# Optimization experiments

Hardware: AMD Instinct MI355X
Metric: run time of the kernel (lower is better)

The kernel has to match this reference:

```python
import jax, jax.numpy as jnp
import numpy as np


def setup_inputs() -> dict:
    key = jax.random.key(0)
    k1, k2 = jax.random.split(key)
    B, C, H, W = 8, 16, 512, 512
    x = jax.random.normal(k1, (B, C, H, W), dtype=jnp.float32)
    # displacement field in voxel units, channels-first like the torch module
    phi = jax.random.normal(k2, (B, 2, H, W), dtype=jnp.float32) * 3.0
    return {"x": x, "phi": phi}


def _pull2d_wrap(img, disp):
    """img: [B,H,W,C], disp: [B,H,W,2] (displacement in voxels).
    Linear interpolation with circulant ('dft') boundary = wrap via mod."""
    B, H, W, C = img.shape
    gy = jnp.arange(H, dtype=img.dtype)[:, None]   # [H,1]
    gx = jnp.arange(W, dtype=img.dtype)[None, :]   # [1,W]
    cy = disp[..., 0] + gy                          # [B,H,W] sample coords (abs)
    cx = disp[..., 1] + gx
    y0f = jnp.floor(cy)
    x0f = jnp.floor(cx)
    wy = (cy - y0f)[..., None]                      # [B,H,W,1]
    wx = (cx - x0f)[..., None]
    y0 = jnp.mod(y0f.astype(jnp.int32), H)
    x0 = jnp.mod(x0f.astype(jnp.int32), W)
    y1 = jnp.mod(y0 + 1, H)
    x1 = jnp.mod(x0 + 1, W)

    def gather(im, yi, xi):                         # im [H,W,C]; yi,xi [H,W]
        return im[yi, xi]

    g = jax.vmap(gather)
    v00 = g(img, y0, x0)
    v01 = g(img, y0, x1)
    v10 = g(img, y1, x0)
    v11 = g(img, y1, x1)
    top = v00 * (1 - wx) + v01 * wx
    bot = v10 * (1 - wx) + v11 * wx
    return top * (1 - wy) + bot * wy                # [B,H,W,C]


def reference(x, phi):
    # x: [B,C,H,W], phi: [B,2,H,W] -> channels-last, pull, channels-first
    img = jnp.moveaxis(x, 1, -1)
    disp = jnp.moveaxis(phi, 1, -1)
    out = _pull2d_wrap(img, disp)
    return jnp.moveaxis(out, -1, 1)
```

## Files before the change

### kernel.cpp

```cpp
#include <hip/hip_runtime.h>


constexpr int B = 8, C = 16, H = 512, W = 512;
constexpr int HW = H * W;

typedef float    v2f __attribute__((ext_vector_type(2)));
typedef _Float16 v8h __attribute__((ext_vector_type(8)));

__global__ __launch_bounds__(256) void transpose_h_kernel(const float* __restrict__ x,
                                                          v8h* __restrict__ xt8) {
    int idx = blockIdx.x * blockDim.x + threadIdx.x;
    int b   = idx >> 18;
    int rem = idx & ((1 << 18) - 1);
    int pp  = rem >> 1;
    int q8  = rem & 1;
    int p0  = pp * 2;

    const float* src = x + ((size_t)b * C + q8 * 8) * HW + p0;
    v8h o0, o1;
#pragma unroll
    for (int j = 0; j < 8; ++j) {
        v2f c = __builtin_nontemporal_load((const v2f*)(src + (size_t)j * HW));
        o0[j] = (_Float16)c.x;
        o1[j] = (_Float16)c.y;
    }

    v8h* dst = xt8 + ((size_t)b * HW + p0) * 2 + q8;
    dst[0] = o0;
    dst[2] = o1;
}

__global__ __launch_bounds__(256) void gather_h_kernel(const v8h* __restrict__ xt8,
                                                       const float* __restrict__ phi,
                                                       float* __restrict__ out) {
    int idx = blockIdx.x * blockDim.x + threadIdx.x;
    int b   = idx >> 19;
    int rem = idx & (HW * 2 - 1);
    int p   = rem >> 1;
    int q   = rem & 1;
    int h   = p >> 9;
    int w   = p & (W - 1);

    const float* phib = phi + (size_t)b * 2 * HW;
    float cy = __builtin_nontemporal_load(phib + p)      + (float)h;
    float cx = __builtin_nontemporal_load(phib + HW + p) + (float)w;

    float y0f = floorf(cy);
    float x0f = floorf(cx);
    float wy  = cy - y0f;
    float wx  = cx - x0f;

    int y0 = ((int)y0f) & (H - 1);
    int x0 = ((int)x0f) & (W - 1);
    int y1 = (y0 + 1)   & (H - 1);
    int x1 = (x0 + 1)   & (W - 1);

    const v8h* base = xt8 + (size_t)b * HW * 2;
    v8h v00 = base[(y0 * W + x0) * 2 + q];
    v8h v01 = base[(y0 * W + x1) * 2 + q];
    v8h v10 = base[(y1 * W + x0) * 2 + q];
    v8h v11 = base[(y1 * W + x1) * 2 + q];

    float omwx = 1.0f - wx;
    float omwy = 1.0f - wy;

    float* outp = out + ((size_t)b * C + q * 8) * HW + p;
#pragma unroll
    for (int j = 0; j < 8; ++j) {
        float top = (float)v00[j] * omwx + (float)v01[j] * wx;
        float bot = (float)v10[j] * omwx + (float)v11[j] * wx;
        __builtin_nontemporal_store(top * omwy + bot * wy, outp + (size_t)j * HW);
    }
}

__global__ __launch_bounds__(256) void pull_wrap_kernel(const float* __restrict__ x,
                                                        const float* __restrict__ phi,
                                                        float* __restrict__ out) {
    int idx = blockIdx.x * blockDim.x + threadIdx.x;
    if (idx >= B * HW) return;
    int b  = idx >> 18;
    int hw = idx & (HW - 1);
    int h  = hw >> 9;
    int w  = hw & (W - 1);

    const float* phib = phi + (size_t)b * 2 * HW;
    float cy = phib[hw]      + (float)h;
    float cx = phib[HW + hw] + (float)w;

    float y0f = floorf(cy);
    float x0f = floorf(cx);
    float wy  = cy - y0f;
    float wx  = cx - x0f;

    int y0 = ((int)y0f) & (H - 1);
    int x0 = ((int)x0f) & (W - 1);
    int y1 = (y0 + 1)   & (H - 1);
    int x1 = (x0 + 1)   & (W - 1);

    int o00 = y0 * W + x0;
    int o01 = y0 * W + x1;
    int o10 = y1 * W + x0;
    int o11 = y1 * W + x1;

    float omwx = 1.0f - wx;
    float omwy = 1.0f - wy;

    const float* plane = x   + (size_t)b * C * HW;
    float*       outp  = out + (size_t)b * C * HW + hw;

#pragma unroll
    for (int c = 0; c < C; ++c) {
        float v00 = plane[o00];
        float v01 = plane[o01];
        float v10 = plane[o10];
        float v11 = plane[o11];
        float top = v00 * omwx + v01 * wx;
        float bot = v10 * omwx + v11 * wx;
        outp[(size_t)c * HW] = top * omwy + bot * wy;
        plane += HW;
    }
}

extern "C" void kernel_launch(void* const* d_in, const int* in_sizes, int n_in,
                              void* d_out, int out_size, void* d_ws, size_t ws_size,
                              hipStream_t stream) {
    const float* x   = (const float*)d_in[0];
    const float* phi = (const float*)d_in[1];
    float* out = (float*)d_out;

    size_t need = (size_t)B * HW * C * sizeof(_Float16);
    if (d_ws != nullptr && ws_size >= need) {
        dim3 block(256);
        dim3 tgrid((B * (HW / 2) * 2) / 256);
        dim3 ggrid((B * HW * 2) / 256);
        transpose_h_kernel<<<tgrid, block, 0, stream>>>(x, (v8h*)d_ws);
        gather_h_kernel<<<ggrid, block, 0, stream>>>((const v8h*)d_ws, phi, out);
    } else {
        int n = B * HW;
        dim3 block(256);
        dim3 grid((n + 255) / 256);
        pull_wrap_kernel<<<grid, block, 0, stream>>>(x, phi, out);
    }
}
```

Before: 274.4 us.

## Widen transpose to 4 pixels, gather all 16 channels per thread, add XCD swizzle

The transpose kernel now loads float4 and emits four fp16 channel vectors per thread, halving its thread count. The gather kernel has each thread handle all 16 channels of one pixel, so the coordinate and weight math and the phi loads are not repeated across two threads. Both kernels remap block IDs so contiguous work chunks land on the same XCD, which should improve L2 locality for the gathers. Each gather thread now holds more registers and issues more loads, which may reduce occupancy.

```diff
diff --git a/kernel.cpp b/kernel.cpp
--- a/kernel.cpp
+++ b/kernel.cpp
@@ -3,41 +3,51 @@
 
 constexpr int B = 8, C = 16, H = 512, W = 512;
 constexpr int HW = H * W;
+constexpr int NXCD = 8;
 
-typedef float    v2f __attribute__((ext_vector_type(2)));
+typedef float    v4f __attribute__((ext_vector_type(4)));
 typedef _Float16 v8h __attribute__((ext_vector_type(8)));
 
-__global__ __launch_bounds__(256) void transpose_h_kernel(const float* __restrict__ x,
-                                                          v8h* __restrict__ xt8) {
-    int idx = blockIdx.x * blockDim.x + threadIdx.x;
-    int b   = idx >> 18;
-    int rem = idx & ((1 << 18) - 1);
+template <int CPX>
+__device__ __forceinline__ int swz(int bid) {
+    return (bid & (NXCD - 1)) * CPX + (bid >> 3);
+}
+
+__global__ __launch_bounds__(256) void transpose_h4_kernel(const float* __restrict__ x,
+                                                           v8h* __restrict__ xt8) {
+    constexpr int CPX = (B * (HW / 4) * 2 / 256) / NXCD;
+    int idx = swz<CPX>((int)blockIdx.x) * 256 + (int)threadIdx.x;
+    int b   = idx >> 17;
+    int rem = idx & ((1 << 17) - 1);
     int pp  = rem >> 1;
     int q8  = rem & 1;
-    int p0  = pp * 2;
+    int p0  = pp * 4;
 
     const float* src = x + ((size_t)b * C + q8 * 8) * HW + p0;
-    v8h o0, o1;
+    v8h o0, o1, o2, o3;
 #pragma unroll
     for (int j = 0; j < 8; ++j) {
-        v2f c = __builtin_nontemporal_load((const v2f*)(src + (size_t)j * HW));
+        v4f c = __builtin_nontemporal_load((const v4f*)(src + (size_t)j * HW));
         o0[j] = (_Float16)c.x;
         o1[j] = (_Float16)c.y;
+        o2[j] = (_Float16)c.z;
+        o3[j] = (_Float16)c.w;
     }
 
     v8h* dst = xt8 + ((size_t)b * HW + p0) * 2 + q8;
     dst[0] = o0;
     dst[2] = o1;
+    dst[4] = o2;
+    dst[6] = o3;
 }
 
-__global__ __launch_bounds__(256) void gather_h_kernel(const v8h* __restrict__ xt8,
-                                                       const float* __restrict__ phi,
-                                                       float* __restrict__ out) {
-    int idx = blockIdx.x * blockDim.x + threadIdx.x;
-    int b   = idx >> 19;
-    int rem = idx & (HW * 2 - 1);
-    int p   = rem >> 1;
-    int q   = rem & 1;
+__global__ __launch_bounds__(256) void gather_h1_kernel(const v8h* __restrict__ xt8,
+                                                        const float* __restrict__ phi,
+                                                        float* __restrict__ out) {
+    constexpr int CPX = (B * HW / 256) / NXCD;
+    int idx = swz<CPX>((int)blockIdx.x) * 256 + (int)threadIdx.x;
+    int b   = idx >> 18;
+    int p   = idx & (HW - 1);
     int h   = p >> 9;
     int w   = p & (W - 1);
 
@@ -56,20 +66,30 @@
     int x1 = (x0 + 1)   & (W - 1);
 
     const v8h* base = xt8 + (size_t)b * HW * 2;
-    v8h v00 = base[(y0 * W + x0) * 2 + q];
-    v8h v01 = base[(y0 * W + x1) * 2 + q];
-    v8h v10 = base[(y1 * W + x0) * 2 + q];
-    v8h v11 = base[(y1 * W + x1) * 2 + q];
+    int o00 = (y0 * W + x0) * 2;
+    int o01 = (y0 * W + x1) * 2;
+    int o10 = (y1 * W + x0) * 2;
+    int o11 = (y1 * W + x1) * 2;
+    v8h a00 = base[o00], b00 = base[o00 + 1];
+    v8h a01 = base[o01], b01 = base[o01 + 1];
+    v8h a10 = base[o10], b10 = base[o10 + 1];
+    v8h a11 = base[o11], b11 = base[o11 + 1];
 
     float omwx = 1.0f - wx;
     float omwy = 1.0f - wy;
 
-    float* outp = out + ((size_t)b * C + q * 8) * HW + p;
+    float* outp = out + (size_t)b * C * HW + p;
 #pragma unroll
     for (int j = 0; j < 8; ++j) {
-        float top = (float)v00[j] * omwx + (float)v01[j] * wx;
-        float bot = (float)v10[j] * omwx + (float)v11[j] * wx;
+        float top = (float)a00[j] * omwx + (float)a01[j] * wx;
+        float bot = (float)a10[j] * omwx + (float)a11[j] * wx;
         __builtin_nontemporal_store(top * omwy + bot * wy, outp + (size_t)j * HW);
+    }
+#pragma unroll
+    for (int j = 0; j < 8; ++j) {
+        float top = (float)b00[j] * omwx + (float)b01[j] * wx;
+        float bot = (float)b10[j] * omwx + (float)b11[j] * wx;
+        __builtin_nontemporal_store(top * omwy + bot * wy, outp + (size_t)(8 + j) * HW);
     }
 }
 
@@ -131,10 +151,10 @@
     size_t need = (size_t)B * HW * C * sizeof(_Float16);
     if (d_ws != nullptr && ws_size >= need) {
         dim3 block(256);
-        dim3 tgrid((B * (HW / 2) * 2) / 256);
-        dim3 ggrid((B * HW * 2) / 256);
-        transpose_h_kernel<<<tgrid, block, 0, stream>>>(x, (v8h*)d_ws);
-        gather_h_kernel<<<ggrid, block, 0, stream>>>((const v8h*)d_ws, phi, out);
+        dim3 tgrid((B * (HW / 4) * 2) / 256);
+        dim3 ggrid((B * HW) / 256);
+        transpose_h4_kernel<<<tgrid, block, 0, stream>>>(x, (v8h*)d_ws);
+        gather_h1_kernel<<<ggrid, block, 0, stream>>>((const v8h*)d_ws, phi, out);
     } else {
         int n = B * HW;
         dim3 block(256);
```

Result: slower. 287.6 us (+4.8%).
